# Performance work log

Hardware: AMD Instinct MI355X
Metric: run time of the kernel (lower is better)

## Reference

```python
import jax, jax.numpy as jnp
import numpy as np

MARGIN = 1.0


def setup_inputs() -> dict:
    key = jax.random.key(0)
    k1, k2, k3 = jax.random.split(key, 3)
    n, d = 8192, 128
    feat1 = jax.random.normal(k1, (n, d), dtype=jnp.float32)
    feat2 = jax.random.normal(k2, (n, d), dtype=jnp.float32)
    # similarity labels in {+1, -1}, as expected by HingeEmbeddingLoss
    simi = (2 * jax.random.randint(k3, (n, n), 0, 2) - 1).astype(jnp.int32)
    return {"feat1": feat1, "feat2": feat2, "simi": simi}


def reference(feat1, feat2, simi):
    # logits[i,j] = -||feat1_i - feat2_j||^2, computed without the O(n*m*d) expand
    sq1 = jnp.sum(feat1 * feat1, axis=-1, keepdims=True)          # [n, 1]
    sq2 = jnp.sum(feat2 * feat2, axis=-1)                          # [m]
    cross = jnp.einsum('nd,md->nm', feat1, feat2)                  # [n, m]
    logits = -(sq1 + sq2[None, :] - 2.0 * cross)                   # [n, m]
    probs = jax.nn.softmax(logits, axis=1)                         # [n, m]
    # HingeEmbeddingLoss: x if y==1 else max(0, margin - x); mean reduction
    loss = jnp.where(simi == 1, probs, jnp.maximum(0.0, MARGIN - probs))
    return jnp.mean(loss)
```

## Files before the change

### kernel.cpp

```cpp
#include <hip/hip_runtime.h>
#include <hip/hip_bf16.h>
#include <stdint.h>

#define N 8192
#define D 128
#define NCHUNK 16
#define CHUNK (N / NCHUNK)
#define RT 128
#define CT 64
#define NTILES (CHUNK / CT)

typedef short bf16x8 __attribute__((ext_vector_type(8)));
typedef float f32x4 __attribute__((ext_vector_type(4)));
typedef unsigned int uint32;
typedef unsigned long long uint64;

#define OFF_ACC   0u
#define OFF_SQ2   1024u
#define OFF_RPOS  (OFF_SQ2 + N * 4u)
#define OFF_M     (OFF_RPOS + N * 4u)
#define OFF_L     (OFF_M + NCHUNK * N * 4u)
#define OFF_S     (OFF_L + NCHUNK * N * 4u)
#define OFF_F1    (OFF_S + NCHUNK * N * 4u)
#define OFF_F2    (OFF_F1 + N * D * 2u)
#define OFF_PACK  (OFF_F2 + N * D * 2u)

__global__ __launch_bounds__(256)
void prep_kernel(const float* __restrict__ f1, const float* __restrict__ f2,
                 unsigned short* __restrict__ f1b, unsigned short* __restrict__ f2b,
                 float* __restrict__ sq2) {
    const int w    = blockIdx.x * 4 + (threadIdx.x >> 6);
    const int lane = threadIdx.x & 63;
    for (int row = w; row < N; row += 1024) {
        float a0 = f1[row * D + lane];
        float a1 = f1[row * D + 64 + lane];
        float b0 = f2[row * D + lane];
        float b1 = f2[row * D + 64 + lane];
        __hip_bfloat16 t;
        t = __float2bfloat16(a0); f1b[row * D + lane]      = *(unsigned short*)&t;
        t = __float2bfloat16(a1); f1b[row * D + 64 + lane] = *(unsigned short*)&t;
        t = __float2bfloat16(b0); f2b[row * D + lane]      = *(unsigned short*)&t;
        t = __float2bfloat16(b1); f2b[row * D + 64 + lane] = *(unsigned short*)&t;
        float ss = b0 * b0 + b1 * b1;
        #pragma unroll
        for (int off = 32; off > 0; off >>= 1) ss += __shfl_xor(ss, off);
        if (lane == 0) sq2[row] = ss;
    }
}

__global__ __launch_bounds__(256)
void pack_kernel(const int* __restrict__ simi, uint64* __restrict__ packed,
                 uint32* __restrict__ rowpos) {
    const int wave = threadIdx.x >> 6;
    const int lane = threadIdx.x & 63;
    const int row  = blockIdx.x * 4 + wave;
    const int* rp = simi + (size_t)row * N;
    uint64* dstrow = packed + (size_t)row * (N / 64);
    uint32 pos = 0;
    #pragma unroll 2
    for (int seg = 0; seg < N / 256; seg++) {
        const int cb = seg * 256;
        int v0 = rp[cb + lane];
        int v1 = rp[cb + 64 + lane];
        int v2 = rp[cb + 128 + lane];
        int v3 = rp[cb + 192 + lane];
        uint64 b0 = __ballot(v0 == 1);
        uint64 b1 = __ballot(v1 == 1);
        uint64 b2 = __ballot(v2 == 1);
        uint64 b3 = __ballot(v3 == 1);
        if (lane == 0) {
            ulonglong2 p01 = {b0, b1}, p23 = {b2, b3};
            *reinterpret_cast<ulonglong2*>(dstrow + seg * 4)     = p01;
            *reinterpret_cast<ulonglong2*>(dstrow + seg * 4 + 2) = p23;
            pos += (uint32)(__popcll(b0) + __popcll(b1) + __popcll(b2) + __popcll(b3));
        }
    }
    if (lane == 0) rowpos[row] = pos;
}

__global__ __launch_bounds__(256)
void main_kernel(const unsigned short* __restrict__ f1b,
                 const unsigned short* __restrict__ f2b,
                 const float* __restrict__ sq2,
                 const uint32* __restrict__ packed32,
                 float* __restrict__ pm, float* __restrict__ pl, float* __restrict__ ps) {
    __shared__ unsigned short ldsB[CT * D];
    __shared__ float ldsSq[CHUNK];

    const int tid  = threadIdx.x;
    const int wave = tid >> 6;
    const int lane = tid & 63;
    const int lo   = lane & 15;
    const int hi   = lane >> 4;

    const int rowtile = blockIdx.x;
    const int chunk   = blockIdx.y;
    const int rbase   = rowtile * RT + wave * 32;
    const int cbase0  = chunk * CHUNK;

    for (int i = tid; i < CHUNK; i += 256) ldsSq[i] = sq2[cbase0 + i];

    bf16x8 afrag[2][4];
    #pragma unroll
    for (int a = 0; a < 2; a++) {
        const unsigned short* ap = f1b + (size_t)(rbase + a * 16 + lo) * D + hi * 8;
        #pragma unroll
        for (int kk = 0; kk < 4; kk++)
            afrag[a][kk] = *reinterpret_cast<const bf16x8*>(ap + kk * 32);
    }

    const int sq_ = (tid >> 4);
    const int sg_ = tid & 15;

    const uint32* pk = packed32 + (size_t)(rbase + hi * 4) * (N / 32)
                                + (cbase0 >> 5) + (lo >> 3);
    const int mshift = 4 * (lo & 7);

    float m[2][4], l[2][4], s[2][4];
    #pragma unroll
    for (int a = 0; a < 2; a++)
        #pragma unroll
        for (int r = 0; r < 4; r++) { m[a][r] = -1e30f; l[a][r] = 0.f; s[a][r] = 0.f; }

    for (int t = 0; t < NTILES; t++) {
        const int cbase = cbase0 + t * CT;

        uint32 mb[2][4];
        #pragma unroll
        for (int a = 0; a < 2; a++)
            #pragma unroll
            for (int r = 0; r < 4; r++)
                mb[a][r] = (pk[(size_t)(a * 16 + r) * (N / 32)] >> mshift) & 0xfu;

        __syncthreads();
        #pragma unroll
        for (int it = 0; it < 4; it++) {
            int q = it * 16 + sq_;
            int c = 4 * (q & 15) + (q >> 4);
            const uint4 v = *reinterpret_cast<const uint4*>(f2b + (size_t)(cbase + c) * D + sg_ * 8);
            *reinterpret_cast<uint4*>(ldsB + q * D + ((sg_ ^ (q & 15)) * 8)) = v;
        }
        __syncthreads();

        f32x4 acc[2][4];
        #pragma unroll
        for (int cf = 0; cf < 4; cf++) {
            acc[0][cf] = (f32x4){0.f, 0.f, 0.f, 0.f};
            acc[1][cf] = (f32x4){0.f, 0.f, 0.f, 0.f};
            const int brow = cf * 16 + lo;
            #pragma unroll
            for (int kk = 0; kk < 4; kk++) {
                int g = kk * 4 + hi;
                bf16x8 b = *reinterpret_cast<const bf16x8*>(
                    ldsB + brow * D + ((g ^ (brow & 15)) * 8));
                acc[0][cf] = __builtin_amdgcn_mfma_f32_16x16x32_bf16(afrag[0][kk], b, acc[0][cf], 0, 0, 0);
                acc[1][cf] = __builtin_amdgcn_mfma_f32_16x16x32_bf16(afrag[1][kk], b, acc[1][cf], 0, 0, 0);
            }
        }

        f32x4 sqv = *reinterpret_cast<const f32x4*>(&ldsSq[t * CT + 4 * lo]);
        #pragma unroll
        for (int a = 0; a < 2; a++) {
            #pragma unroll
            for (int cf = 0; cf < 4; cf++)
                #pragma unroll
                for (int r = 0; r < 4; r++)
                    acc[a][cf][r] = 2.0f * acc[a][cf][r] - sqv[cf];

            #pragma unroll
            for (int r = 0; r < 4; r++) {
                float tm = fmaxf(fmaxf(acc[a][0][r], acc[a][1][r]),
                                 fmaxf(acc[a][2][r], acc[a][3][r]));
                #pragma unroll
                for (int off = 1; off < 16; off <<= 1)
                    tm = fmaxf(tm, __shfl_xor(tm, off));
                float mn = fmaxf(m[a][r], tm);
                float al = __expf(m[a][r] - mn);
                l[a][r] *= al; s[a][r] *= al; m[a][r] = mn;
            }
            #pragma unroll
            for (int r = 0; r < 4; r++)
                #pragma unroll
                for (int cf = 0; cf < 4; cf++) {
                    float p = __expf(acc[a][cf][r] - m[a][r]);
                    l[a][r] += p;
                    if ((mb[a][r] >> cf) & 1u) s[a][r] += p;
                }
        }
        pk += 2;
    }

    #pragma unroll
    for (int a = 0; a < 2; a++) {
        #pragma unroll
        for (int r = 0; r < 4; r++) {
            #pragma unroll
            for (int off = 1; off < 16; off <<= 1) {
                l[a][r] += __shfl_xor(l[a][r], off);
                s[a][r] += __shfl_xor(s[a][r], off);
            }
        }
    }
    if (lo == 0) {
        #pragma unroll
        for (int a = 0; a < 2; a++)
            #pragma unroll
            for (int r = 0; r < 4; r++) {
                int row = rbase + a * 16 + hi * 4 + r;
                int idx = chunk * N + row;
                pm[idx] = m[a][r]; pl[idx] = l[a][r]; ps[idx] = s[a][r];
            }
    }
}

__global__ void merge_kernel(const float* __restrict__ pm, const float* __restrict__ pl,
                             const float* __restrict__ ps, const uint32* __restrict__ rowpos,
                             float* __restrict__ s_acc, uint32* __restrict__ pos_acc) {
    const int row = blockIdx.x * 256 + threadIdx.x;
    float M = -1e30f;
    #pragma unroll
    for (int k = 0; k < NCHUNK; k++) M = fmaxf(M, pm[k * N + row]);
    float L = 0.f, S = 0.f;
    #pragma unroll
    for (int k = 0; k < NCHUNK; k++) {
        float e = __expf(pm[k * N + row] - M);
        L += pl[k * N + row] * e;
        S += ps[k * N + row] * e;
    }
    float r = S / L;
    uint32 pc = rowpos[row];
    #pragma unroll
    for (int off = 32; off > 0; off >>= 1) {
        r  += __shfl_xor(r, off);
        pc += __shfl_xor(pc, off);
    }
    __shared__ float red[4];
    __shared__ uint32 redp[4];
    int lane = threadIdx.x & 63, w = threadIdx.x >> 6;
    if (lane == 0) { red[w] = r; redp[w] = pc; }
    __syncthreads();
    if (threadIdx.x == 0) {
        atomicAdd(s_acc, red[0] + red[1] + red[2] + red[3]);
        atomicAdd(pos_acc, redp[0] + redp[1] + redp[2] + redp[3]);
    }
}

__global__ void final_kernel(const float* __restrict__ s_acc, const uint32* __restrict__ pos_acc,
                             float* __restrict__ out) {
    double S = (double)s_acc[0];
    double C = (double)N * (double)N - (double)pos_acc[0];
    double n = (double)N;
    out[0] = (float)((2.0 * S + C - n) / (n * n));
}

extern "C" void kernel_launch(void* const* d_in, const int* in_sizes, int n_in,
                              void* d_out, int out_size, void* d_ws, size_t ws_size,
                              hipStream_t stream) {
    const float* f1   = (const float*)d_in[0];
    const float* f2   = (const float*)d_in[1];
    const int*   simi = (const int*)d_in[2];
    float* out = (float*)d_out;
    char* ws = (char*)d_ws;

    float*  acc_s  = (float*)(ws + OFF_ACC);
    uint32* acc_p  = (uint32*)(ws + OFF_ACC + 4);
    float*  sq2    = (float*)(ws + OFF_SQ2);
    uint32* rowpos = (uint32*)(ws + OFF_RPOS);
    float*  pm     = (float*)(ws + OFF_M);
    float*  pl     = (float*)(ws + OFF_L);
    float*  ps     = (float*)(ws + OFF_S);
    unsigned short* f1b = (unsigned short*)(ws + OFF_F1);
    unsigned short* f2b = (unsigned short*)(ws + OFF_F2);
    uint64* packed = (uint64*)(ws + OFF_PACK);

    hipMemsetAsync(ws + OFF_ACC, 0, 64, stream);
    prep_kernel<<<256, 256, 0, stream>>>(f1, f2, f1b, f2b, sq2);
    pack_kernel<<<N / 4, 256, 0, stream>>>(simi, packed, rowpos);
    main_kernel<<<dim3(N / RT, NCHUNK), 256, 0, stream>>>(f1b, f2b, sq2,
                                                          (const uint32*)packed, pm, pl, ps);
    merge_kernel<<<N / 256, 256, 0, stream>>>(pm, pl, ps, rowpos, acc_s, acc_p);
    final_kernel<<<1, 1, 0, stream>>>(acc_s, acc_p, out);
}
```

Baseline: 434.5 us.

## Drop LDS staging of B tiles, keep per-lane softmax max, deepen pack prefetch

The main kernel no longer stages feat2 tiles and sq2 in shared memory behind two barriers per tile. Each lane now loads its B fragments and sq2 values straight from global memory, relying on the cache, since every wave in a block reads the same columns. The online softmax keeps a running max per lane and only combines across the 16 lanes once at the end, which removes the per-tile shuffle reductions but can mean more exp rescaling per lane. The pack kernel also preloads 16 values per lane and prefetches the next group to add memory-level parallelism, at the cost of more registers.

```diff
diff --git a/kernel.cpp b/kernel.cpp
--- a/kernel.cpp
+++ b/kernel.cpp
@@ -57,22 +57,31 @@
     const int* rp = simi + (size_t)row * N;
     uint64* dstrow = packed + (size_t)row * (N / 64);
     uint32 pos = 0;
-    #pragma unroll 2
-    for (int seg = 0; seg < N / 256; seg++) {
-        const int cb = seg * 256;
-        int v0 = rp[cb + lane];
-        int v1 = rp[cb + 64 + lane];
-        int v2 = rp[cb + 128 + lane];
-        int v3 = rp[cb + 192 + lane];
-        uint64 b0 = __ballot(v0 == 1);
-        uint64 b1 = __ballot(v1 == 1);
-        uint64 b2 = __ballot(v2 == 1);
-        uint64 b3 = __ballot(v3 == 1);
+    int v[16];
+    #pragma unroll
+    for (int i = 0; i < 16; i++) v[i] = rp[i * 64 + lane];
+    #pragma unroll
+    for (int g = 0; g < 8; g++) {
+        int w[16];
+        if (g < 7) {
+            #pragma unroll
+            for (int i = 0; i < 16; i++) w[i] = rp[(g + 1) * 1024 + i * 64 + lane];
+        }
+        uint64 b[16];
+        #pragma unroll
+        for (int i = 0; i < 16; i++) b[i] = __ballot(v[i] == 1);
         if (lane == 0) {
-            ulonglong2 p01 = {b0, b1}, p23 = {b2, b3};
-            *reinterpret_cast<ulonglong2*>(dstrow + seg * 4)     = p01;
-            *reinterpret_cast<ulonglong2*>(dstrow + seg * 4 + 2) = p23;
-            pos += (uint32)(__popcll(b0) + __popcll(b1) + __popcll(b2) + __popcll(b3));
+            #pragma unroll
+            for (int i = 0; i < 8; i++) {
+                ulonglong2 p = {b[2 * i], b[2 * i + 1]};
+                *reinterpret_cast<ulonglong2*>(dstrow + g * 16 + 2 * i) = p;
+            }
+            #pragma unroll
+            for (int i = 0; i < 16; i++) pos += (uint32)__popcll(b[i]);
+        }
+        if (g < 7) {
+            #pragma unroll
+            for (int i = 0; i < 16; i++) v[i] = w[i];
         }
     }
     if (lane == 0) rowpos[row] = pos;
@@ -84,9 +93,6 @@
                  const float* __restrict__ sq2,
                  const uint32* __restrict__ packed32,
                  float* __restrict__ pm, float* __restrict__ pl, float* __restrict__ ps) {
-    __shared__ unsigned short ldsB[CT * D];
-    __shared__ float ldsSq[CHUNK];
-
     const int tid  = threadIdx.x;
     const int wave = tid >> 6;
     const int lane = tid & 63;
@@ -98,8 +104,6 @@
     const int rbase   = rowtile * RT + wave * 32;
     const int cbase0  = chunk * CHUNK;
 
-    for (int i = tid; i < CHUNK; i += 256) ldsSq[i] = sq2[cbase0 + i];
-
     bf16x8 afrag[2][4];
     #pragma unroll
     for (int a = 0; a < 2; a++) {
@@ -108,14 +112,13 @@
         for (int kk = 0; kk < 4; kk++)
             afrag[a][kk] = *reinterpret_cast<const bf16x8*>(ap + kk * 32);
     }
-
-    const int sq_ = (tid >> 4);
-    const int sg_ = tid & 15;
 
     const uint32* pk = packed32 + (size_t)(rbase + hi * 4) * (N / 32)
                                 + (cbase0 >> 5) + (lo >> 3);
     const int mshift = 4 * (lo & 7);
 
+    const unsigned short* bp = f2b + (size_t)(cbase0 + 4 * lo) * D + hi * 8;
+
     float m[2][4], l[2][4], s[2][4];
     #pragma unroll
     for (int a = 0; a < 2; a++)
@@ -123,94 +126,74 @@
         for (int r = 0; r < 4; r++) { m[a][r] = -1e30f; l[a][r] = 0.f; s[a][r] = 0.f; }
 
     for (int t = 0; t < NTILES; t++) {
-        const int cbase = cbase0 + t * CT;
-
         uint32 mb[2][4];
         #pragma unroll
         for (int a = 0; a < 2; a++)
             #pragma unroll
             for (int r = 0; r < 4; r++)
                 mb[a][r] = (pk[(size_t)(a * 16 + r) * (N / 32)] >> mshift) & 0xfu;
-
-        __syncthreads();
-        #pragma unroll
-        for (int it = 0; it < 4; it++) {
-            int q = it * 16 + sq_;
-            int c = 4 * (q & 15) + (q >> 4);
-            const uint4 v = *reinterpret_cast<const uint4*>(f2b + (size_t)(cbase + c) * D + sg_ * 8);
-            *reinterpret_cast<uint4*>(ldsB + q * D + ((sg_ ^ (q & 15)) * 8)) = v;
-        }
-        __syncthreads();
 
         f32x4 acc[2][4];
         #pragma unroll
         for (int cf = 0; cf < 4; cf++) {
             acc[0][cf] = (f32x4){0.f, 0.f, 0.f, 0.f};
             acc[1][cf] = (f32x4){0.f, 0.f, 0.f, 0.f};
-            const int brow = cf * 16 + lo;
+            const unsigned short* bc = bp + (size_t)(t * CT + cf) * D;
             #pragma unroll
             for (int kk = 0; kk < 4; kk++) {
-                int g = kk * 4 + hi;
-                bf16x8 b = *reinterpret_cast<const bf16x8*>(
-                    ldsB + brow * D + ((g ^ (brow & 15)) * 8));
+                bf16x8 b = *reinterpret_cast<const bf16x8*>(bc + kk * 32);
                 acc[0][cf] = __builtin_amdgcn_mfma_f32_16x16x32_bf16(afrag[0][kk], b, acc[0][cf], 0, 0, 0);
                 acc[1][cf] = __builtin_amdgcn_mfma_f32_16x16x32_bf16(afrag[1][kk], b, acc[1][cf], 0, 0, 0);
             }
         }
 
-        f32x4 sqv = *reinterpret_cast<const f32x4*>(&ldsSq[t * CT + 4 * lo]);
-        #pragma unroll
-        for (int a = 0; a < 2; a++) {
-            #pragma unroll
-            for (int cf = 0; cf < 4; cf++)
+        f32x4 sqv = *reinterpret_cast<const f32x4*>(sq2 + cbase0 + t * CT + 4 * lo);
+        #pragma unroll
+        for (int a = 0; a < 2; a++)
+            #pragma unroll
+            for (int r = 0; r < 4; r++) {
+                float lg[4];
                 #pragma unroll
-                for (int r = 0; r < 4; r++)
-                    acc[a][cf][r] = 2.0f * acc[a][cf][r] - sqv[cf];
-
-            #pragma unroll
-            for (int r = 0; r < 4; r++) {
-                float tm = fmaxf(fmaxf(acc[a][0][r], acc[a][1][r]),
-                                 fmaxf(acc[a][2][r], acc[a][3][r]));
-                #pragma unroll
-                for (int off = 1; off < 16; off <<= 1)
-                    tm = fmaxf(tm, __shfl_xor(tm, off));
+                for (int cf = 0; cf < 4; cf++)
+                    lg[cf] = 2.0f * acc[a][cf][r] - sqv[cf];
+                float tm = fmaxf(fmaxf(lg[0], lg[1]), fmaxf(lg[2], lg[3]));
                 float mn = fmaxf(m[a][r], tm);
                 float al = __expf(m[a][r] - mn);
-                l[a][r] *= al; s[a][r] *= al; m[a][r] = mn;
-            }
-            #pragma unroll
-            for (int r = 0; r < 4; r++)
+                m[a][r] = mn;
+                float p[4];
                 #pragma unroll
-                for (int cf = 0; cf < 4; cf++) {
-                    float p = __expf(acc[a][cf][r] - m[a][r]);
-                    l[a][r] += p;
-                    if ((mb[a][r] >> cf) & 1u) s[a][r] += p;
-                }
-        }
+                for (int cf = 0; cf < 4; cf++) p[cf] = __expf(lg[cf] - mn);
+                l[a][r] = l[a][r] * al + ((p[0] + p[1]) + (p[2] + p[3]));
+                float sm = 0.f;
+                #pragma unroll
+                for (int cf = 0; cf < 4; cf++)
+                    sm += ((mb[a][r] >> cf) & 1u) ? p[cf] : 0.f;
+                s[a][r] = s[a][r] * al + sm;
+            }
         pk += 2;
     }
 
     #pragma unroll
-    for (int a = 0; a < 2; a++) {
+    for (int a = 0; a < 2; a++)
         #pragma unroll
         for (int r = 0; r < 4; r++) {
+            float M = m[a][r];
+            #pragma unroll
+            for (int off = 1; off < 16; off <<= 1)
+                M = fmaxf(M, __shfl_xor(M, off));
+            float sc = __expf(m[a][r] - M);
+            float L = l[a][r] * sc, S = s[a][r] * sc;
             #pragma unroll
             for (int off = 1; off < 16; off <<= 1) {
-                l[a][r] += __shfl_xor(l[a][r], off);
-                s[a][r] += __shfl_xor(s[a][r], off);
-            }
-        }
-    }
-    if (lo == 0) {
-        #pragma unroll
-        for (int a = 0; a < 2; a++)
-            #pragma unroll
-            for (int r = 0; r < 4; r++) {
+                L += __shfl_xor(L, off);
+                S += __shfl_xor(S, off);
+            }
+            if (lo == 0) {
                 int row = rbase + a * 16 + hi * 4 + r;
                 int idx = chunk * N + row;
-                pm[idx] = m[a][r]; pl[idx] = l[a][r]; ps[idx] = s[a][r];
-            }
-    }
+                pm[idx] = M; pl[idx] = L; ps[idx] = S;
+            }
+        }
 }
 
 __global__ void merge_kernel(const float* __restrict__ pm, const float* __restrict__ pl,
```

After: 450.6 us. +3.7%, slower.
